# Kernel optimization log

Measured on AMD Instinct MI355X. Metric: run time of the kernel, lower is better.

## Reference

```python
import jax, jax.numpy as jnp
import numpy as np

EPS = 1e-12  # F.normalize eps

def _unfold3(x):
    # x: [B,C,H,W] -> [B, C*9, H*W], matching F.unfold(kernel=3, padding=1)
    B, C, H, W = x.shape
    xp = jnp.pad(x, ((0, 0), (0, 0), (1, 1), (1, 1)))
    pats = jnp.stack([xp[:, :, i:i + H, j:j + W]
                      for i in range(3) for j in range(3)], axis=2)  # [B,C,9,H,W]
    return pats.reshape(B, C * 9, H * W)

def _fold3(t, H, W):
    # inverse of _unfold3 with overlap-add, matching F.fold(kernel=3, padding=1)
    B, CK, L = t.shape
    C = CK // 9
    t = t.reshape(B, C, 3, 3, H, W)
    out = jnp.zeros((B, C, H + 2, W + 2), t.dtype)
    for i in range(3):
        for j in range(3):
            out = out.at[:, :, i:i + H, j:j + W].add(t[:, :, i, j])
    return out[:, :, 1:1 + H, 1:1 + W]

def setup_inputs() -> dict:
    key = jax.random.key(0)
    kV, kK, kQ = jax.random.split(key, 3)
    B, C, H, W = 4, 64, 64, 64
    return {
        'V': jax.random.normal(kV, (B, C, H, W), dtype=jnp.float32),
        'K': jax.random.normal(kK, (B, C, H, W), dtype=jnp.float32),
        'Q': jax.random.normal(kQ, (B, C, H, W), dtype=jnp.float32),
    }

def reference(V, K, Q):
    B, C, H, W = Q.shape
    Qu = _unfold3(Q)  # [B, C9, L]
    Ku = _unfold3(K)  # [B, C9, L]
    # F.normalize along the feature (C*9) axis for both K (after permute dim=2) and Q (dim=1)
    Kn = Ku / jnp.maximum(jnp.linalg.norm(Ku, axis=1, keepdims=True), EPS)
    Qn = Qu / jnp.maximum(jnp.linalg.norm(Qu, axis=1, keepdims=True), EPS)
    # R[b,k,q] = <Kn[b,:,k], Qn[b,:,q]>  -> [B, L, L]
    R = jnp.einsum('bfk,bfq->bkq', Kn, Qn)
    S = jnp.max(R, axis=1)        # [B, L]
    arg = jnp.argmax(R, axis=1)   # [B, L] best key patch per query position
    Vu = _unfold3(V)              # [B, C9, L]
    idx = jnp.broadcast_to(arg[:, None, :], Vu.shape)
    T_unfold = jnp.take_along_axis(Vu, idx, axis=2)  # gather along patch dim
    T = _fold3(T_unfold, H, W) / 9.0                 # [B, C, H, W]
    S = S.reshape(B, 1, H, W)
    return (S, T)
```

## Files before the change

### kernel.cpp

```cpp
#include <hip/hip_runtime.h>
#include <math.h>

#define HW 4096

typedef short bf16x8 __attribute__((ext_vector_type(8)));
typedef float floatx4 __attribute__((ext_vector_type(4)));
typedef unsigned short u16x8 __attribute__((ext_vector_type(8)));

__device__ __forceinline__ unsigned short f2bf_rne(float x) {
    unsigned int u = __float_as_uint(x);
    unsigned int r = (u + 0x7FFFu + ((u >> 16) & 1u)) >> 16;
    return (unsigned short)r;
}
__device__ __forceinline__ float bf2f(unsigned short h) {
    return __uint_as_float(((unsigned int)h) << 16);
}

__device__ __forceinline__ void gload_lds16(const void* gptr, void* lptr) {
    auto g = (const __attribute__((address_space(1))) unsigned int*)(unsigned long long)(gptr);
    auto l = (__attribute__((address_space(3))) unsigned int*)(unsigned int)(unsigned long long)(lptr);
    __builtin_amdgcn_global_load_lds(g, l, 16, 0, 0);
}

__global__ __launch_bounds__(256)
void prep_kernel(const float* __restrict__ Q, const float* __restrict__ K,
                 const float* __restrict__ V,
                 unsigned short* __restrict__ Aq, unsigned short* __restrict__ Bq,
                 float* __restrict__ VT,
                 float* __restrict__ pix2q, float* __restrict__ pix2k) {
    __shared__ float sT[64][65];
    const int tid = threadIdx.x;
    const int p0 = blockIdx.x * 64;
    const int b = blockIdx.y;
    const int which = blockIdx.z;
    const float* __restrict__ src = (which == 0) ? Q : ((which == 1) ? K : V);

#pragma unroll
    for (int it = 0; it < 16; ++it) {
        int idx = it * 256 + tid;
        int c = idx >> 6, x = idx & 63;
        sT[c][x] = src[((size_t)b * 64 + c) * HW + p0 + x];
    }
    __syncthreads();
    const int pp = tid >> 2, qt = tid & 3;

    if (which == 2) {
        float* dst = VT + ((size_t)b * 4096 + p0 + pp) * 64 + qt * 16;
#pragma unroll
        for (int j = 0; j < 4; ++j) {
            float4 v = make_float4(sT[qt * 16 + 4 * j + 0][pp], sT[qt * 16 + 4 * j + 1][pp],
                                   sT[qt * 16 + 4 * j + 2][pp], sT[qt * 16 + 4 * j + 3][pp]);
            *(float4*)(dst + 4 * j) = v;
        }
        return;
    }

    const int isK = which;
    unsigned short* __restrict__ dst = isK ? Bq : Aq;
    float* __restrict__ pix2 = isK ? pix2k : pix2q;
    const size_t base = ((size_t)b * 4096 + p0 + pp) * 192;
    {
        float sq = 0.f;
        u16x8 hv[2], lv[2];
#pragma unroll
        for (int g = 0; g < 2; ++g)
#pragma unroll
            for (int j = 0; j < 8; ++j) {
                int c = qt * 16 + g * 8 + j;
                float x = sT[c][pp];
                sq = fmaf(x, x, sq);
                unsigned short h = f2bf_rne(x);
                hv[g][j] = h;
                lv[g][j] = f2bf_rne(x - bf2f(h));
            }
        sq += __shfl_xor(sq, 1, 64);
        sq += __shfl_xor(sq, 2, 64);
        if (qt == 0) pix2[(b << 12) + p0 + pp] = sq;
#pragma unroll
        for (int g = 0; g < 2; ++g) {
            int co = qt * 16 + g * 8;
            *(u16x8*)(dst + base + co)                     = hv[g];
            *(u16x8*)(dst + base + (isK ? 64 : 128) + co)  = lv[g];
        }
    }
}

#define WAITV(n_) asm volatile("s_waitcnt vmcnt(" #n_ ")" ::: "memory")
#define PBAR(n_) do { WAITV(n_); __builtin_amdgcn_s_barrier(); \
                      asm volatile("" ::: "memory"); } while (0)
#define SB do { __builtin_amdgcn_s_barrier(); asm volatile("" ::: "memory"); } while (0)

#define ISSUE_A(c_, sg_, slot_) \
    gload_lds16(agb + (size_t)((c_) * 64 + rr) * 384 + (sg_) * 128 + G16, \
                smem + (slot_) * 8192 + t16)
#define ISSUE_B(c_, sg_, slot_) \
    gload_lds16(bgb + (size_t)((c_) * 64 + rr) * 384 + (sg_) * 128 + G16, \
                smemB + (slot_) * 8192 + t16)

#define GISS_A(c_, sg_, slot_) do { \
    uint4 v_ = make_uint4(0u, 0u, 0u, 0u); \
    if ((unsigned)(arow + (c_) * 64 + rr) < 4096u) \
        v_ = *(const uint4*)(agb + (ptrdiff_t)((c_) * 64 + rr) * 384 + (sg_) * 128 + G16); \
    *(uint4*)(smem + (slot_) * 8192 + t16) = v_; \
} while (0)
#define GISS_B(c_, sg_, slot_) do { \
    uint4 v_ = make_uint4(0u, 0u, 0u, 0u); \
    if ((unsigned)(brow + (c_) * 64 + rr) < 4096u) \
        v_ = *(const uint4*)(bgb + (ptrdiff_t)((c_) * 64 + rr) * 384 + (sg_) * 128 + G16); \
    *(uint4*)(smemB + (slot_) * 8192 + t16) = v_; \
} while (0)

#define MM8(af_, bf_) do { \
    __builtin_amdgcn_s_setprio(1); \
    _Pragma("unroll") \
    for (int mt_ = 0; mt_ < 4; ++mt_) \
        _Pragma("unroll") \
        for (int nt_ = 0; nt_ < 2; ++nt_) \
            acc[mt_][nt_] = __builtin_amdgcn_mfma_f32_16x16x32_bf16( \
                (af_)[mt_], (bf_)[nt_], acc[mt_][nt_], 0, 0, 0); \
    __builtin_amdgcn_s_setprio(0); \
} while (0)

#define DY_MEGA(dy_) do { \
    const char* AhS_ = smem + ahS[wm + (dy_)] * 8192 + rowB; \
    const char* AlS_ = smem + alS[wm + (dy_)] * 8192 + rowB; \
    const char* BhS_ = smemB + bhS[wnC + (dy_)] * 8192 + rowBB; \
    const char* BlS_ = smemB + blS[wnC + (dy_)] * 8192 + rowBB; \
    _Pragma("unroll 1") \
    for (int kk = 0; kk < 2; ++kk) { \
        const int pk_ = kk ? posK1 : posK0; \
        bf16x8 afc[4], bfc[2], t4[4]; \
        _Pragma("unroll") \
        for (int mt = 0; mt < 4; ++mt) \
            afc[mt] = *(const bf16x8*)(AhS_ + mt * 2048 + pk_); \
        _Pragma("unroll") \
        for (int nt = 0; nt < 2; ++nt) \
            bfc[nt] = *(const bf16x8*)(BhS_ + nt * 2048 + pk_); \
        MM8(afc, bfc); \
        _Pragma("unroll") \
        for (int nt = 0; nt < 2; ++nt) \
            t4[nt] = *(const bf16x8*)(BlS_ + nt * 2048 + pk_); \
        MM8(afc, t4); \
        _Pragma("unroll") \
        for (int mt = 0; mt < 4; ++mt) \
            t4[mt] = *(const bf16x8*)(AlS_ + mt * 2048 + pk_); \
        MM8(t4, bfc); \
    } \
} while (0)

__global__ __launch_bounds__(512, 4)
void gemm_fused_kernel(const unsigned short* __restrict__ Aq, const unsigned short* __restrict__ Bq,
                       const float* __restrict__ pix2k,
                       float* __restrict__ part_val, int* __restrict__ part_arg) {
    __shared__ __align__(16) char smem[81920];
    char* const smemB = smem + 40960;
    const int tid = threadIdx.x;
    const int lane = tid & 63, wid = tid >> 6;
    const int m15 = lane & 15, quad = lane >> 4;
    const int wm = wid & 1;
    const int wn2 = wid >> 1;
    const int wnC = wn2 >> 1, wnF = wn2 & 1;
    const int ahS[4] = {0, 1, 4, 2};
    const int alS[4] = {2, 3, 0, 3};
    const int bhS[4] = {0, 1, 4, 2};
    const int blS[4] = {2, 3, 0, 3};
    const int f = blockIdx.x + (blockIdx.y << 5);
    const int o = ((f & 7) << 7) + (f >> 3);
    const int kt = o & 31, qt = o >> 5;
    const int k0 = kt << 7;
    const int q0 = qt << 7;
    const int b = blockIdx.z;
    const int arow = q0 - 64, brow = k0 - 64;
    const char* agb = (const char*)(Aq + (size_t)b * 4096 * 192) + (ptrdiff_t)arow * 384;
    const char* bgb = (const char*)(Bq + (size_t)b * 4096 * 192) + (ptrdiff_t)brow * 384;
    const bool aInt = (q0 >= 64) && (q0 <= 4096 - 192);
    const bool bInt = (k0 >= 64) && (k0 <= 4096 - 192);

    const int rr = tid >> 3;
    const int G16 = ((tid & 7) ^ (rr & 7)) * 16;
    const int t16 = tid * 16;
    const int rowB = m15 * 128;
    const int rowBB = (wnF * 32 + m15) * 128;
    const int posK0 = (quad ^ (m15 & 7)) * 16;
    const int posK1 = ((4 + quad) ^ (m15 & 7)) * 16;

    floatx4 acc[4][2];
#pragma unroll
    for (int i = 0; i < 4; ++i)
#pragma unroll
        for (int j = 0; j < 2; ++j) acc[i][j] = (floatx4)0.f;

    if (aInt && bInt) {
        ISSUE_A(0, 0, 0); ISSUE_A(1, 0, 1); ISSUE_B(0, 0, 0); ISSUE_B(1, 0, 1);
        ISSUE_A(0, 2, 2); ISSUE_A(1, 2, 3); ISSUE_B(0, 1, 2); ISSUE_B(1, 1, 3);
        ISSUE_A(2, 0, 4); ISSUE_B(2, 0, 4);
        PBAR(2);
        DY_MEGA(0);
        SB;
        ISSUE_A(2, 2, 0);
        ISSUE_B(2, 1, 0);
        ISSUE_A(3, 0, 2);
        ISSUE_B(3, 0, 2);
        PBAR(2);
        DY_MEGA(1);
        SB;
        ISSUE_A(3, 2, 3);
        ISSUE_B(3, 1, 3);
        PBAR(0);
        DY_MEGA(2);
    } else {
        GISS_A(0, 0, 0); GISS_A(1, 0, 1); GISS_B(0, 0, 0); GISS_B(1, 0, 1);
        GISS_A(0, 2, 2); GISS_A(1, 2, 3); GISS_B(0, 1, 2); GISS_B(1, 1, 3);
        GISS_A(2, 0, 4); GISS_B(2, 0, 4);
        __syncthreads();
        DY_MEGA(0);
        __syncthreads();
        GISS_A(2, 2, 0); GISS_B(2, 1, 0); GISS_A(3, 0, 2); GISS_B(3, 0, 2);
        __syncthreads();
        DY_MEGA(1);
        __syncthreads();
        GISS_A(3, 2, 3); GISS_B(3, 1, 3);
        __syncthreads();
        DY_MEGA(2);
    }
    __syncthreads();

    float* Csh = (float*)smem;
    float* bvs = (float*)(smem + 34816);
    int*   bas = (int*)(smem + 36864);
    float* Lrnk = (float*)(smem + 38912);
    if (tid < 128) {
        int k = k0 + tid;
        int py = k >> 6, px = k & 63;
        float sk = 0.f;
        for (int dy = -1; dy <= 1; ++dy)
            for (int dx = -1; dx <= 1; ++dx) {
                int yy = py + dy, xx = px + dx;
                if ((unsigned)yy < 64u && (unsigned)xx < 64u)
                    sk += pix2k[(b << 12) + (yy << 6) + xx];
            }
        Lrnk[tid] = 1.f / fmaxf(sqrtf(sk), 1e-12f);
    }
    const int q_l = tid & 63;
    const int qr = tid >> 6;
    const int c0 = qr * 16;
    const float4 zero4 = make_float4(0.f, 0.f, 0.f, 0.f);

#pragma unroll
    for (int h = 0; h < 2; ++h) {
        if (h) __syncthreads();
        if (wm == h) {
#pragma unroll
            for (int mt = 0; mt < 4; ++mt)
#pragma unroll
                for (int nt = 0; nt < 2; ++nt)
#pragma unroll
                    for (int j = 0; j < 4; ++j)
                        Csh[(mt * 16 + quad * 4 + j) * 133 + (wn2 << 5) + nt * 16 + m15] =
                            acc[mt][nt][j];
        }
        __syncthreads();

        const bool qm = q_l > 0;
        const bool qp = q_l < 63;
        const float* rC = Csh + q_l * 133;
        const float* rM = Csh + (q_l - 1) * 133;
        const float* rP = Csh + (q_l + 1) * 133;
        float4 prevm = (qm && c0 > 0) ? *(const float4*)&rM[c0 - 4] : zero4;
        float4 rpj   = qp ? *(const float4*)&rP[c0] : zero4;
        float bv = -INFINITY;
        int ba = 0;
#pragma unroll
        for (int j = 0; j < 4; ++j) {
            int c = c0 + 4 * j;
            float4 cen = *(const float4*)&rC[c];
            float4 rm4 = qm ? *(const float4*)&rM[c] : zero4;
            float4 rp1 = (qp && (c + 4) < 128) ? *(const float4*)&rP[c + 4] : zero4;
            float4 o4;
            o4.x = cen.x + (((c & 63) != 0) ? prevm.w : 0.f) + rpj.y;
            o4.y = cen.y + rm4.x + rpj.z;
            o4.z = cen.z + rm4.y + rpj.w;
            o4.w = cen.w + rm4.z + ((((c + 3) & 63) != 63) ? rp1.x : 0.f);
            float4 rk = *(const float4*)&Lrnk[c];
            float v0 = o4.x * rk.x; if (v0 > bv) { bv = v0; ba = k0 + c + 0; }
            float v1 = o4.y * rk.y; if (v1 > bv) { bv = v1; ba = k0 + c + 1; }
            float v2 = o4.z * rk.z; if (v2 > bv) { bv = v2; ba = k0 + c + 2; }
            float v3 = o4.w * rk.w; if (v3 > bv) { bv = v3; ba = k0 + c + 3; }
            prevm = rm4;
            rpj = rp1;
        }
        bvs[(qr << 6) + q_l] = bv;
        bas[(qr << 6) + q_l] = ba;
        __syncthreads();
        if (tid < 64) {
            float v = bvs[tid];
            int a = bas[tid];
#pragma unroll
            for (int s = 1; s < 8; ++s) {
                float v2 = bvs[(s << 6) + tid];
                if (v2 > v) { v = v2; a = bas[(s << 6) + tid]; }
            }
            int q = q0 + h * 64 + tid;
            part_val[(((b << 5) + kt) << 12) + q] = v;
            part_arg[(((b << 5) + kt) << 12) + q] = a;
        }
    }
}

__global__ __launch_bounds__(256)
void argcombine_kernel(const float* __restrict__ part_val, const int* __restrict__ part_arg,
                       const float* __restrict__ pix2q,
                       float* __restrict__ S_out, int* __restrict__ argF) {
    __shared__ float rv[4][64];
    __shared__ int ra[4][64];
    const int tid = threadIdx.x;
    const int qi = tid & 63, sg = tid >> 6;
    const int q = blockIdx.x * 64 + qi;
    const int b = blockIdx.y;
    const int base = (b << 17) + q;
    float bv = -INFINITY; int ba = 0;
#pragma unroll
    for (int i = 0; i < 8; ++i) {
        int s = sg * 8 + i;
        float v = part_val[base + (s << 12)];
        int aa = part_arg[base + (s << 12)];
        if (v > bv) { bv = v; ba = aa; }
    }
    rv[sg][qi] = bv; ra[sg][qi] = ba;
    __syncthreads();
    if (tid < 64) {
        float v = rv[0][tid]; int a = ra[0][tid];
#pragma unroll
        for (int s = 1; s < 4; ++s) {
            float v2 = rv[s][tid];
            if (v2 > v) { v = v2; a = ra[s][tid]; }
        }
        int py = blockIdx.x, px = tid;
        float sq = 0.f;
        for (int dy = -1; dy <= 1; ++dy)
            for (int dx = -1; dx <= 1; ++dx) {
                int y2 = py + dy, x2 = px + dx;
                if ((unsigned)y2 < 64u && (unsigned)x2 < 64u)
                    sq += pix2q[(b << 12) + (y2 << 6) + x2];
            }
        int idx = (b << 12) + (py << 6) + px;
        S_out[idx] = v * (1.f / fmaxf(sqrtf(sq), 1e-12f));
        argF[idx] = a;
    }
}

__global__ __launch_bounds__(256)
void gatherT_kernel(const float* __restrict__ VT, const int* __restrict__ argF,
                    float* __restrict__ T_out) {
    __shared__ int sArg[192];
    const int y = blockIdx.x, b = blockIdx.y, cg = blockIdx.z;
    const int tid = threadIdx.x;
    if (tid < 192) {
        int r = tid >> 6, x = tid & 63;
        int yy = y - 1 + r;
        sArg[tid] = ((unsigned)yy < 64u) ? argF[(b << 12) + (yy << 6) + x] : 0;
    }
    __syncthreads();

    const int x = tid >> 2, cq = tid & 3;
    const float* Vb = VT + (size_t)b * 4096 * 64 + cg * 16 + cq * 4;
    float ax = 0.f, ay = 0.f, az = 0.f, aw = 0.f;
#pragma unroll
    for (int t = 0; t < 9; ++t) {
        int dy = t / 3 - 1, dx = t % 3 - 1;
        int qy = y - dy, qx = x - dx;
        if ((unsigned)qy < 64u && (unsigned)qx < 64u) {
            int a = sArg[(1 - dy) * 64 + qx];
            int sy = (a >> 6) + dy, sx = (a & 63) + dx;
            if ((unsigned)sy < 64u && (unsigned)sx < 64u) {
                float4 v = *(const float4*)(Vb + (size_t)((sy << 6) + sx) * 64);
                ax += v.x; ay += v.y; az += v.z; aw += v.w;
            }
        }
    }
    float* Tb = T_out + ((size_t)b * 64 + cg * 16 + cq * 4) * HW + (y << 6) + x;
    Tb[0]          = ax * (1.f / 9.f);
    Tb[HW]         = ay * (1.f / 9.f);
    Tb[2 * HW]     = az * (1.f / 9.f);
    Tb[3 * HW]     = aw * (1.f / 9.f);
}

extern "C" void kernel_launch(void* const* d_in, const int* in_sizes, int n_in,
                              void* d_out, int out_size, void* d_ws, size_t ws_size,
                              hipStream_t stream) {
    const float* V = (const float*)d_in[0];
    const float* K = (const float*)d_in[1];
    const float* Q = (const float*)d_in[2];
    float* S_out = (float*)d_out;
    float* T_out = S_out + 4 * HW;

    char* ws = (char*)d_ws;
    float* pix2q = (float*)(ws + 0);
    float* pix2k = (float*)(ws + 65536);
    float* part_val = (float*)(ws + 262144);
    int*   argF  = (int*)(ws + 4456448);
    int*   part_arg = (int*)(ws + 8650752);
    float* VT    = (float*)(ws + 10747904);
    unsigned short* Aq = (unsigned short*)(ws + 17039360);
    unsigned short* Bq = (unsigned short*)(ws + 23330816);

    prep_kernel<<<dim3(64, 4, 3), 256, 0, stream>>>(Q, K, V, Aq, Bq, VT, pix2q, pix2k);
    gemm_fused_kernel<<<dim3(32, 32, 4), 512, 0, stream>>>(Aq, Bq, pix2k, part_val, part_arg);
    argcombine_kernel<<<dim3(64, 4), 256, 0, stream>>>(part_val, part_arg, pix2q, S_out, argF);
    gatherT_kernel<<<dim3(64, 4, 4), 256, 0, stream>>>(VT, argF, T_out);
}
```

Baseline: 190.5 us.

## Loop each GEMM block over eight key tiles and fold argcombine into gather

The GEMM grid shrinks from 4096 blocks, one per query/key tile pair, to 512 blocks. Each block now loops over eight key tiles, carries a running max and argmax in registers, and writes only four partials per query. The separate argcombine kernel is removed: the gather kernel reduces the four partials and writes S directly, which saves a launch and cuts partial-buffer traffic. The MFMA inner loop is also restructured so all fragment loads are issued before a single prioritized block of MFMAs with the kk loop unrolled. The trade-off is fewer blocks, which may underfill 256 CUs with 512 blocks, plus serialized per-tile epilogues inside each block.

```diff
diff --git a/kernel.cpp b/kernel.cpp
--- a/kernel.cpp
+++ b/kernel.cpp
@@ -111,14 +111,12 @@
 } while (0)
 
 #define MM8(af_, bf_) do { \
-    __builtin_amdgcn_s_setprio(1); \
     _Pragma("unroll") \
     for (int mt_ = 0; mt_ < 4; ++mt_) \
         _Pragma("unroll") \
         for (int nt_ = 0; nt_ < 2; ++nt_) \
             acc[mt_][nt_] = __builtin_amdgcn_mfma_f32_16x16x32_bf16( \
                 (af_)[mt_], (bf_)[nt_], acc[mt_][nt_], 0, 0, 0); \
-    __builtin_amdgcn_s_setprio(0); \
 } while (0)
 
 #define DY_MEGA(dy_) do { \
@@ -126,25 +124,27 @@
     const char* AlS_ = smem + alS[wm + (dy_)] * 8192 + rowB; \
     const char* BhS_ = smemB + bhS[wnC + (dy_)] * 8192 + rowBB; \
     const char* BlS_ = smemB + blS[wnC + (dy_)] * 8192 + rowBB; \
-    _Pragma("unroll 1") \
+    _Pragma("unroll") \
     for (int kk = 0; kk < 2; ++kk) { \
         const int pk_ = kk ? posK1 : posK0; \
-        bf16x8 afc[4], bfc[2], t4[4]; \
+        bf16x8 afc[4], bfc[2], bl2[2], al4[4]; \
         _Pragma("unroll") \
         for (int mt = 0; mt < 4; ++mt) \
             afc[mt] = *(const bf16x8*)(AhS_ + mt * 2048 + pk_); \
         _Pragma("unroll") \
         for (int nt = 0; nt < 2; ++nt) \
             bfc[nt] = *(const bf16x8*)(BhS_ + nt * 2048 + pk_); \
-        MM8(afc, bfc); \
         _Pragma("unroll") \
         for (int nt = 0; nt < 2; ++nt) \
-            t4[nt] = *(const bf16x8*)(BlS_ + nt * 2048 + pk_); \
-        MM8(afc, t4); \
+            bl2[nt] = *(const bf16x8*)(BlS_ + nt * 2048 + pk_); \
         _Pragma("unroll") \
         for (int mt = 0; mt < 4; ++mt) \
-            t4[mt] = *(const bf16x8*)(AlS_ + mt * 2048 + pk_); \
-        MM8(t4, bfc); \
+            al4[mt] = *(const bf16x8*)(AlS_ + mt * 2048 + pk_); \
+        __builtin_amdgcn_s_setprio(1); \
+        MM8(afc, bfc); \
+        MM8(afc, bl2); \
+        MM8(al4, bfc); \
+        __builtin_amdgcn_s_setprio(0); \
     } \
 } while (0)
 
@@ -164,17 +164,15 @@
     const int alS[4] = {2, 3, 0, 3};
     const int bhS[4] = {0, 1, 4, 2};
     const int blS[4] = {2, 3, 0, 3};
-    const int f = blockIdx.x + (blockIdx.y << 5);
-    const int o = ((f & 7) << 7) + (f >> 3);
-    const int kt = o & 31, qt = o >> 5;
-    const int k0 = kt << 7;
+    const int f = blockIdx.x;
+    const int o = ((f & 7) << 4) + (f >> 3);
+    const int qt = o >> 2, kQ = o & 3;
     const int q0 = qt << 7;
-    const int b = blockIdx.z;
-    const int arow = q0 - 64, brow = k0 - 64;
+    const int b = blockIdx.y;
+    const int arow = q0 - 64;
     const char* agb = (const char*)(Aq + (size_t)b * 4096 * 192) + (ptrdiff_t)arow * 384;
-    const char* bgb = (const char*)(Bq + (size_t)b * 4096 * 192) + (ptrdiff_t)brow * 384;
+    const char* Bqb = (const char*)(Bq + (size_t)b * 4096 * 192);
     const bool aInt = (q0 >= 64) && (q0 <= 4096 - 192);
-    const bool bInt = (k0 >= 64) && (k0 <= 4096 - 192);
 
     const int rr = tid >> 3;
     const int G16 = ((tid & 7) ^ (rr & 7)) * 16;
@@ -184,113 +182,130 @@
     const int posK0 = (quad ^ (m15 & 7)) * 16;
     const int posK1 = ((4 + quad) ^ (m15 & 7)) * 16;
 
-    floatx4 acc[4][2];
-#pragma unroll
-    for (int i = 0; i < 4; ++i)
-#pragma unroll
-        for (int j = 0; j < 2; ++j) acc[i][j] = (floatx4)0.f;
-
-    if (aInt && bInt) {
-        ISSUE_A(0, 0, 0); ISSUE_A(1, 0, 1); ISSUE_B(0, 0, 0); ISSUE_B(1, 0, 1);
-        ISSUE_A(0, 2, 2); ISSUE_A(1, 2, 3); ISSUE_B(0, 1, 2); ISSUE_B(1, 1, 3);
-        ISSUE_A(2, 0, 4); ISSUE_B(2, 0, 4);
-        PBAR(2);
-        DY_MEGA(0);
-        SB;
-        ISSUE_A(2, 2, 0);
-        ISSUE_B(2, 1, 0);
-        ISSUE_A(3, 0, 2);
-        ISSUE_B(3, 0, 2);
-        PBAR(2);
-        DY_MEGA(1);
-        SB;
-        ISSUE_A(3, 2, 3);
-        ISSUE_B(3, 1, 3);
-        PBAR(0);
-        DY_MEGA(2);
-    } else {
-        GISS_A(0, 0, 0); GISS_A(1, 0, 1); GISS_B(0, 0, 0); GISS_B(1, 0, 1);
-        GISS_A(0, 2, 2); GISS_A(1, 2, 3); GISS_B(0, 1, 2); GISS_B(1, 1, 3);
-        GISS_A(2, 0, 4); GISS_B(2, 0, 4);
-        __syncthreads();
-        DY_MEGA(0);
-        __syncthreads();
-        GISS_A(2, 2, 0); GISS_B(2, 1, 0); GISS_A(3, 0, 2); GISS_B(3, 0, 2);
-        __syncthreads();
-        DY_MEGA(1);
-        __syncthreads();
-        GISS_A(3, 2, 3); GISS_B(3, 1, 3);
-        __syncthreads();
-        DY_MEGA(2);
-    }
-    __syncthreads();
-
     float* Csh = (float*)smem;
     float* bvs = (float*)(smem + 34816);
     int*   bas = (int*)(smem + 36864);
     float* Lrnk = (float*)(smem + 38912);
-    if (tid < 128) {
-        int k = k0 + tid;
-        int py = k >> 6, px = k & 63;
-        float sk = 0.f;
-        for (int dy = -1; dy <= 1; ++dy)
-            for (int dx = -1; dx <= 1; ++dx) {
-                int yy = py + dy, xx = px + dx;
-                if ((unsigned)yy < 64u && (unsigned)xx < 64u)
-                    sk += pix2k[(b << 12) + (yy << 6) + xx];
-            }
-        Lrnk[tid] = 1.f / fmaxf(sqrtf(sk), 1e-12f);
-    }
     const int q_l = tid & 63;
     const int qr = tid >> 6;
     const int c0 = qr * 16;
     const float4 zero4 = make_float4(0.f, 0.f, 0.f, 0.f);
 
+    float bvr[2] = {-INFINITY, -INFINITY};
+    int   bar[2] = {0, 0};
+
+    for (int t = 0; t < 8; ++t) {
+        const int k0 = (kQ << 10) + (t << 7);
+        const int brow = k0 - 64;
+        const char* bgb = Bqb + (ptrdiff_t)brow * 384;
+        const bool bInt = (k0 >= 64) && (k0 <= 4096 - 192);
+
+        floatx4 acc[4][2];
+#pragma unroll
+        for (int i = 0; i < 4; ++i)
+#pragma unroll
+            for (int j = 0; j < 2; ++j) acc[i][j] = (floatx4)0.f;
+
+        if (aInt && bInt) {
+            ISSUE_A(0, 0, 0); ISSUE_A(1, 0, 1); ISSUE_B(0, 0, 0); ISSUE_B(1, 0, 1);
+            ISSUE_A(0, 2, 2); ISSUE_A(1, 2, 3); ISSUE_B(0, 1, 2); ISSUE_B(1, 1, 3);
+            ISSUE_A(2, 0, 4); ISSUE_B(2, 0, 4);
+            PBAR(2);
+            DY_MEGA(0);
+            SB;
+            ISSUE_A(2, 2, 0);
+            ISSUE_B(2, 1, 0);
+            ISSUE_A(3, 0, 2);
+            ISSUE_B(3, 0, 2);
+            PBAR(2);
+            DY_MEGA(1);
+            SB;
+            ISSUE_A(3, 2, 3);
+            ISSUE_B(3, 1, 3);
+            PBAR(0);
+            DY_MEGA(2);
+        } else {
+            GISS_A(0, 0, 0); GISS_A(1, 0, 1); GISS_B(0, 0, 0); GISS_B(1, 0, 1);
+            GISS_A(0, 2, 2); GISS_A(1, 2, 3); GISS_B(0, 1, 2); GISS_B(1, 1, 3);
+            GISS_A(2, 0, 4); GISS_B(2, 0, 4);
+            __syncthreads();
+            DY_MEGA(0);
+            __syncthreads();
+            GISS_A(2, 2, 0); GISS_B(2, 1, 0); GISS_A(3, 0, 2); GISS_B(3, 0, 2);
+            __syncthreads();
+            DY_MEGA(1);
+            __syncthreads();
+            GISS_A(3, 2, 3); GISS_B(3, 1, 3);
+            __syncthreads();
+            DY_MEGA(2);
+        }
+        __syncthreads();
+
+        if (tid < 128) {
+            int k = k0 + tid;
+            int py = k >> 6, px = k & 63;
+            float sk = 0.f;
+            for (int dy = -1; dy <= 1; ++dy)
+                for (int dx = -1; dx <= 1; ++dx) {
+                    int yy = py + dy, xx = px + dx;
+                    if ((unsigned)yy < 64u && (unsigned)xx < 64u)
+                        sk += pix2k[(b << 12) + (yy << 6) + xx];
+                }
+            Lrnk[tid] = 1.f / fmaxf(sqrtf(sk), 1e-12f);
+        }
+#pragma unroll
+        for (int h = 0; h < 2; ++h) {
+            if (h) __syncthreads();
+            if (wm == h) {
+#pragma unroll
+                for (int mt = 0; mt < 4; ++mt)
+#pragma unroll
+                    for (int nt = 0; nt < 2; ++nt)
+#pragma unroll
+                        for (int j = 0; j < 4; ++j)
+                            Csh[(mt * 16 + quad * 4 + j) * 133 + (wn2 << 5) + nt * 16 + m15] =
+                                acc[mt][nt][j];
+            }
+            __syncthreads();
+
+            const bool qm = q_l > 0;
+            const bool qp = q_l < 63;
+            const float* rC = Csh + q_l * 133;
+            const float* rM = Csh + (q_l - 1) * 133;
+            const float* rP = Csh + (q_l + 1) * 133;
+            float4 prevm = (qm && c0 > 0) ? *(const float4*)&rM[c0 - 4] : zero4;
+            float4 rpj   = qp ? *(const float4*)&rP[c0] : zero4;
+            float bv = bvr[h];
+            int ba = bar[h];
+#pragma unroll
+            for (int j = 0; j < 4; ++j) {
+                int c = c0 + 4 * j;
+                float4 cen = *(const float4*)&rC[c];
+                float4 rm4 = qm ? *(const float4*)&rM[c] : zero4;
+                float4 rp1 = (qp && (c + 4) < 128) ? *(const float4*)&rP[c + 4] : zero4;
+                float4 o4;
+                o4.x = cen.x + (((c & 63) != 0) ? prevm.w : 0.f) + rpj.y;
+                o4.y = cen.y + rm4.x + rpj.z;
+                o4.z = cen.z + rm4.y + rpj.w;
+                o4.w = cen.w + rm4.z + ((((c + 3) & 63) != 63) ? rp1.x : 0.f);
+                float4 rk = *(const float4*)&Lrnk[c];
+                float v0 = o4.x * rk.x; if (v0 > bv) { bv = v0; ba = k0 + c + 0; }
+                float v1 = o4.y * rk.y; if (v1 > bv) { bv = v1; ba = k0 + c + 1; }
+                float v2 = o4.z * rk.z; if (v2 > bv) { bv = v2; ba = k0 + c + 2; }
+                float v3 = o4.w * rk.w; if (v3 > bv) { bv = v3; ba = k0 + c + 3; }
+                prevm = rm4;
+                rpj = rp1;
+            }
+            bvr[h] = bv;
+            bar[h] = ba;
+        }
+        __syncthreads();
+    }
+
 #pragma unroll
     for (int h = 0; h < 2; ++h) {
-        if (h) __syncthreads();
-        if (wm == h) {
-#pragma unroll
-            for (int mt = 0; mt < 4; ++mt)
-#pragma unroll
-                for (int nt = 0; nt < 2; ++nt)
-#pragma unroll
-                    for (int j = 0; j < 4; ++j)
-                        Csh[(mt * 16 + quad * 4 + j) * 133 + (wn2 << 5) + nt * 16 + m15] =
-                            acc[mt][nt][j];
-        }
-        __syncthreads();
-
-        const bool qm = q_l > 0;
-        const bool qp = q_l < 63;
-        const float* rC = Csh + q_l * 133;
-        const float* rM = Csh + (q_l - 1) * 133;
-        const float* rP = Csh + (q_l + 1) * 133;
-        float4 prevm = (qm && c0 > 0) ? *(const float4*)&rM[c0 - 4] : zero4;
-        float4 rpj   = qp ? *(const float4*)&rP[c0] : zero4;
-        float bv = -INFINITY;
-        int ba = 0;
-#pragma unroll
-        for (int j = 0; j < 4; ++j) {
-            int c = c0 + 4 * j;
-            float4 cen = *(const float4*)&rC[c];
-            float4 rm4 = qm ? *(const float4*)&rM[c] : zero4;
-            float4 rp1 = (qp && (c + 4) < 128) ? *(const float4*)&rP[c + 4] : zero4;
-            float4 o4;
-            o4.x = cen.x + (((c & 63) != 0) ? prevm.w : 0.f) + rpj.y;
-            o4.y = cen.y + rm4.x + rpj.z;
-            o4.z = cen.z + rm4.y + rpj.w;
-            o4.w = cen.w + rm4.z + ((((c + 3) & 63) != 63) ? rp1.x : 0.f);
-            float4 rk = *(const float4*)&Lrnk[c];
-            float v0 = o4.x * rk.x; if (v0 > bv) { bv = v0; ba = k0 + c + 0; }
-            float v1 = o4.y * rk.y; if (v1 > bv) { bv = v1; ba = k0 + c + 1; }
-            float v2 = o4.z * rk.z; if (v2 > bv) { bv = v2; ba = k0 + c + 2; }
-            float v3 = o4.w * rk.w; if (v3 > bv) { bv = v3; ba = k0 + c + 3; }
-            prevm = rm4;
-            rpj = rp1;
-        }
-        bvs[(qr << 6) + q_l] = bv;
-        bas[(qr << 6) + q_l] = ba;
+        bvs[(qr << 6) + q_l] = bvr[h];
+        bas[(qr << 6) + q_l] = bar[h];
         __syncthreads();
         if (tid < 64) {
             float v = bvs[tid];
@@ -298,67 +313,52 @@
 #pragma unroll
             for (int s = 1; s < 8; ++s) {
                 float v2 = bvs[(s << 6) + tid];
-                if (v2 > v) { v = v2; a = bas[(s << 6) + tid]; }
+                int a2 = bas[(s << 6) + tid];
+                if (v2 > v || (v2 == v && a2 < a)) { v = v2; a = a2; }
             }
             int q = q0 + h * 64 + tid;
-            part_val[(((b << 5) + kt) << 12) + q] = v;
-            part_arg[(((b << 5) + kt) << 12) + q] = a;
-        }
+            part_val[(((b << 2) + kQ) << 12) + q] = v;
+            part_arg[(((b << 2) + kQ) << 12) + q] = a;
+        }
+        __syncthreads();
     }
 }
 
 __global__ __launch_bounds__(256)
-void argcombine_kernel(const float* __restrict__ part_val, const int* __restrict__ part_arg,
-                       const float* __restrict__ pix2q,
-                       float* __restrict__ S_out, int* __restrict__ argF) {
-    __shared__ float rv[4][64];
-    __shared__ int ra[4][64];
-    const int tid = threadIdx.x;
-    const int qi = tid & 63, sg = tid >> 6;
-    const int q = blockIdx.x * 64 + qi;
-    const int b = blockIdx.y;
-    const int base = (b << 17) + q;
-    float bv = -INFINITY; int ba = 0;
-#pragma unroll
-    for (int i = 0; i < 8; ++i) {
-        int s = sg * 8 + i;
-        float v = part_val[base + (s << 12)];
-        int aa = part_arg[base + (s << 12)];
-        if (v > bv) { bv = v; ba = aa; }
-    }
-    rv[sg][qi] = bv; ra[sg][qi] = ba;
-    __syncthreads();
-    if (tid < 64) {
-        float v = rv[0][tid]; int a = ra[0][tid];
-#pragma unroll
-        for (int s = 1; s < 4; ++s) {
-            float v2 = rv[s][tid];
-            if (v2 > v) { v = v2; a = ra[s][tid]; }
-        }
-        int py = blockIdx.x, px = tid;
-        float sq = 0.f;
-        for (int dy = -1; dy <= 1; ++dy)
-            for (int dx = -1; dx <= 1; ++dx) {
-                int y2 = py + dy, x2 = px + dx;
-                if ((unsigned)y2 < 64u && (unsigned)x2 < 64u)
-                    sq += pix2q[(b << 12) + (y2 << 6) + x2];
-            }
-        int idx = (b << 12) + (py << 6) + px;
-        S_out[idx] = v * (1.f / fmaxf(sqrtf(sq), 1e-12f));
-        argF[idx] = a;
-    }
-}
-
-__global__ __launch_bounds__(256)
-void gatherT_kernel(const float* __restrict__ VT, const int* __restrict__ argF,
-                    float* __restrict__ T_out) {
+void gatherT_kernel(const float* __restrict__ VT,
+                    const float* __restrict__ part_val, const int* __restrict__ part_arg,
+                    const float* __restrict__ pix2q,
+                    float* __restrict__ S_out, float* __restrict__ T_out) {
     __shared__ int sArg[192];
     const int y = blockIdx.x, b = blockIdx.y, cg = blockIdx.z;
     const int tid = threadIdx.x;
     if (tid < 192) {
         int r = tid >> 6, x = tid & 63;
         int yy = y - 1 + r;
-        sArg[tid] = ((unsigned)yy < 64u) ? argF[(b << 12) + (yy << 6) + x] : 0;
+        int a = 0;
+        if ((unsigned)yy < 64u) {
+            int base = (b << 14) + (yy << 6) + x;
+            float bv = -INFINITY; int ba = 0;
+#pragma unroll
+            for (int s = 0; s < 4; ++s) {
+                float v = part_val[base + (s << 12)];
+                int aa = part_arg[base + (s << 12)];
+                if (v > bv) { bv = v; ba = aa; }
+            }
+            a = ba;
+            if (r == 1 && cg == 0) {
+                float sq = 0.f;
+                for (int dy = -1; dy <= 1; ++dy)
+                    for (int dx = -1; dx <= 1; ++dx) {
+                        int y2 = yy + dy, x2 = x + dx;
+                        if ((unsigned)y2 < 64u && (unsigned)x2 < 64u)
+                            sq += pix2q[(b << 12) + (y2 << 6) + x2];
+                    }
+                S_out[(b << 12) + (yy << 6) + x] =
+                    bv * (1.f / fmaxf(sqrtf(sq), 1e-12f));
+            }
+        }
+        sArg[tid] = a;
     }
     __syncthreads();
 
@@ -398,14 +398,12 @@
     float* pix2q = (float*)(ws + 0);
     float* pix2k = (float*)(ws + 65536);
     float* part_val = (float*)(ws + 262144);
-    int*   argF  = (int*)(ws + 4456448);
     int*   part_arg = (int*)(ws + 8650752);
     float* VT    = (float*)(ws + 10747904);
     unsigned short* Aq = (unsigned short*)(ws + 17039360);
     unsigned short* Bq = (unsigned short*)(ws + 23330816);
 
     prep_kernel<<<dim3(64, 4, 3), 256, 0, stream>>>(Q, K, V, Aq, Bq, VT, pix2q, pix2k);
-    gemm_fused_kernel<<<dim3(32, 32, 4), 512, 0, stream>>>(Aq, Bq, pix2k, part_val, part_arg);
-    argcombine_kernel<<<dim3(64, 4), 256, 0, stream>>>(part_val, part_arg, pix2q, S_out, argF);
-    gatherT_kernel<<<dim3(64, 4, 4), 256, 0, stream>>>(VT, argF, T_out);
-}
+    gemm_fused_kernel<<<dim3(128, 4), 512, 0, stream>>>(Aq, Bq, pix2k, part_val, part_arg);
+    gatherT_kernel<<<dim3(64, 4, 4), 256, 0, stream>>>(VT, part_val, part_arg, pix2q, S_out, T_out);
+}
```

New measurement: 326.3 us. 1.71x slower.
